# Performance work log

Hardware: AMD Instinct MI355X
Metric: run time of the kernel (lower is better)

Reference implementation:

```python
import jax, jax.numpy as jnp
import numpy as np

HIDDEN = 2048
NUM_HEADS = 16
NUM_KV_HEADS = 8
HEAD_DIM = 128
EPS = 1e-6
ROPE_THETA = 10000.0
SEQ = 2048
Q_SIZE = NUM_HEADS * HEAD_DIM
KV_SIZE = NUM_KV_HEADS * HEAD_DIM


def rmsnorm_f32(x, w, eps=EPS):
    # RMSNormF32: normalize in float32, scale by weight
    xf = x.astype(jnp.float32)
    var = jnp.mean(xf * xf, axis=-1, keepdims=True)
    return xf * jax.lax.rsqrt(var + eps) * w.astype(jnp.float32)


def apply_rope(x, cos, sin):
    # x: [S, H, D]; cos/sin: [S, D//2] (neox-style half split)
    half = x.shape[-1] // 2
    x1, x2 = x[..., :half], x[..., half:]
    c = cos[:, None, :]
    s = sin[:, None, :]
    return jnp.concatenate([x1 * c - x2 * s, x2 * c + x1 * s], axis=-1)


def setup_inputs() -> dict:
    key = jax.random.key(0)
    ks = jax.random.split(key, 6)
    return {
        "positions": jnp.arange(SEQ, dtype=jnp.int32),
        "hidden_states": jax.random.normal(ks[0], (SEQ, HIDDEN), jnp.float32),
        "ln_weight": 1.0 + 0.1 * jax.random.normal(ks[1], (HIDDEN,), jnp.float32),
        "qkv_weight": 0.02 * jax.random.normal(ks[2], (Q_SIZE + 2 * KV_SIZE, HIDDEN), jnp.float32),
        "q_norm_weight": 1.0 + 0.1 * jax.random.normal(ks[3], (HEAD_DIM,), jnp.float32),
        "k_norm_weight": 1.0 + 0.1 * jax.random.normal(ks[4], (HEAD_DIM,), jnp.float32),
        "o_weight": 0.02 * jax.random.normal(ks[5], (HIDDEN, Q_SIZE), jnp.float32),
    }


def reference(positions, hidden_states, ln_weight, qkv_weight, q_norm_weight, k_norm_weight, o_weight):
    S = hidden_states.shape[0]
    # 1. input RMSNorm (f32)
    normalized = rmsnorm_f32(hidden_states, ln_weight)
    # 2. fused QKV projection (no bias)
    qkv = normalized @ qkv_weight.T  # [S, q_size + 2*kv_size]
    q = qkv[:, :Q_SIZE].reshape(S, NUM_HEADS, HEAD_DIM)
    k = qkv[:, Q_SIZE:Q_SIZE + KV_SIZE].reshape(S, NUM_KV_HEADS, HEAD_DIM)
    v = qkv[:, Q_SIZE + KV_SIZE:].reshape(S, NUM_KV_HEADS, HEAD_DIM)
    # 3. RoPE (neox half-split, cache built from theta)
    inv_freq = ROPE_THETA ** (-jnp.arange(0, HEAD_DIM, 2, dtype=jnp.float32) / HEAD_DIM)
    freqs = positions.astype(jnp.float32)[:, None] * inv_freq[None, :]  # [S, D/2]
    cos, sin = jnp.cos(freqs), jnp.sin(freqs)
    q = apply_rope(q, cos, sin)
    k = apply_rope(k, cos, sin)
    # 4. per-head q/k RMSNorm (applied after RoPE, as in source)
    q = rmsnorm_f32(q, q_norm_weight)
    k = rmsnorm_f32(k, k_norm_weight)
    # 5. GQA expand kv heads
    rep = NUM_HEADS // NUM_KV_HEADS
    k = jnp.repeat(k, rep, axis=1)  # [S, NH, D]
    v = jnp.repeat(v, rep, axis=1)
    # 6. naive causal attention
    scores = jnp.einsum('shd,thd->hst', q, k) / (HEAD_DIM ** 0.5)  # [NH, S, S]
    causal = jnp.triu(jnp.ones((S, S), dtype=bool), k=1)
    scores = jnp.where(causal[None, :, :], -jnp.inf, scores)
    attn = jax.nn.softmax(scores, axis=-1)
    attn = jnp.nan_to_num(attn, nan=0.0)
    out = jnp.einsum('hst,thd->shd', attn, v).reshape(S, Q_SIZE)
    # 7. output projection
    return out @ o_weight.T
```

## Files before the change

kernel.cpp:

```cpp
#include <hip/hip_runtime.h>
#include <hip/hip_bf16.h>
#include <stdint.h>

typedef unsigned short u16;
typedef __attribute__((ext_vector_type(4))) float f32x4;
typedef __attribute__((ext_vector_type(8))) __bf16 bf16x8;
typedef __attribute__((ext_vector_type(8))) unsigned short u16x8;

#define SEQ 2048
#define HID 2048
#define HD  128

__device__ __forceinline__ float b2f(u16 v) {
    union { float f; unsigned u; } c; c.u = ((unsigned)v) << 16; return c.f;
}
__device__ __forceinline__ u16 f2b(float f) {
    union { float f; unsigned u; } c; c.f = f;
    unsigned r = c.u + 0x7fffu + ((c.u >> 16) & 1u);
    return (u16)(r >> 16);
}
__device__ __forceinline__ bf16x8 tob(u16x8 v) {
    union { u16x8 u; bf16x8 b; } c; c.u = v; return c.b;
}
__device__ __forceinline__ u16x8 ld8(const u16* p) { return *(const u16x8*)p; }

typedef const __attribute__((address_space(1))) unsigned int* gas_ptr;
typedef __attribute__((address_space(3))) unsigned int* las_ptr;
__device__ __forceinline__ void gld16(const void* g, void* l) {
    __builtin_amdgcn_global_load_lds((gas_ptr)g, (las_ptr)l, 16, 0, 0);
}

__global__ __launch_bounds__(256) void k_conv(const float* __restrict__ src,
                                              u16* __restrict__ dst) {
    const size_t i = ((size_t)blockIdx.x * 256 + threadIdx.x) * 8;
    f32x4 a = *(const f32x4*)(src + i);
    f32x4 b = *(const f32x4*)(src + i + 4);
    u16x8 o;
#pragma unroll
    for (int e = 0; e < 4; ++e) { o[e] = f2b(a[e]); o[e + 4] = f2b(b[e]); }
    *(u16x8*)(dst + i) = o;
}

__global__ __launch_bounds__(256) void k_rmsnorm(const float* __restrict__ x,
                                                 const float* __restrict__ w,
                                                 u16* __restrict__ o) {
    const int row = blockIdx.x, t = threadIdx.x;
    const float* xr = x + (size_t)row * HID + t * 8;
    f32x4 xa = *(const f32x4*)xr;
    f32x4 xb = *(const f32x4*)(xr + 4);
    float xf[8]; float ss = 0.f;
#pragma unroll
    for (int e = 0; e < 4; ++e) { xf[e] = xa[e]; xf[e + 4] = xb[e]; }
#pragma unroll
    for (int e = 0; e < 8; ++e) ss += xf[e] * xf[e];
#pragma unroll
    for (int m = 32; m; m >>= 1) ss += __shfl_xor(ss, m);
    __shared__ float red[4];
    if ((t & 63) == 0) red[t >> 6] = ss;
    __syncthreads();
    ss = red[0] + red[1] + red[2] + red[3];
    const float sc = rsqrtf(ss * (1.0f / HID) + 1e-6f);
    f32x4 wa = *(const f32x4*)(w + t * 8);
    f32x4 wb = *(const f32x4*)(w + t * 8 + 4);
    u16x8 ov;
#pragma unroll
    for (int e = 0; e < 4; ++e) {
        ov[e] = f2b(xf[e] * sc * wa[e]);
        ov[e + 4] = f2b(xf[e + 4] * sc * wb[e]);
    }
    *(u16x8*)(o + (size_t)row * HID + t * 8) = ov;
}

__global__ __launch_bounds__(256) void k_gemm_qkv(const u16* __restrict__ A,
                                                  const u16* __restrict__ B,
                                                  u16* __restrict__ qraw,
                                                  u16* __restrict__ kraw,
                                                  u16* __restrict__ vtr,
                                                  int K) {
    __shared__ u16 As[128 * 32];
    __shared__ u16 Bs[128 * 32];
    const int tid = threadIdx.x;
    const int wave = tid >> 6, lane = tid & 63, quad = lane >> 4, l16 = lane & 15;
    const int wm = wave >> 1, wn = wave & 1;
    const int m0 = blockIdx.x * 128, n0 = blockIdx.y * 128;
    f32x4 acc[4][4];
#pragma unroll
    for (int i = 0; i < 4; ++i)
#pragma unroll
        for (int j = 0; j < 4; ++j) acc[i][j] = (f32x4){0.f, 0.f, 0.f, 0.f};

    const u16* ga = A + (size_t)(m0 + (tid >> 2)) * K + (tid & 3) * 8;
    const u16* gb = B + (size_t)(n0 + (tid >> 2)) * K + (tid & 3) * 8;
    const size_t rowskip = (size_t)64 * K;
    char* lA = (char*)As + wave * 1024;
    char* lB = (char*)Bs + wave * 1024;

    for (int k0 = 0; k0 < K; k0 += 32) {
        gld16(ga + k0, lA);
        gld16(ga + k0 + rowskip, lA + 4096);
        gld16(gb + k0, lB);
        gld16(gb + k0 + rowskip, lB + 4096);
        __syncthreads();
        bf16x8 af[4], bfr[4];
#pragma unroll
        for (int i = 0; i < 4; ++i)
            af[i] = tob(ld8(As + (wm * 64 + i * 16 + l16) * 32 + quad * 8));
#pragma unroll
        for (int j = 0; j < 4; ++j)
            bfr[j] = tob(ld8(Bs + (wn * 64 + j * 16 + l16) * 32 + quad * 8));
#pragma unroll
        for (int i = 0; i < 4; ++i)
#pragma unroll
            for (int j = 0; j < 4; ++j)
                acc[i][j] = __builtin_amdgcn_mfma_f32_16x16x32_bf16(af[i], bfr[j], acc[i][j], 0, 0, 0);
        __syncthreads();
    }
#pragma unroll
    for (int i = 0; i < 4; ++i) {
        const int row = m0 + wm * 64 + i * 16 + quad * 4;
#pragma unroll
        for (int j = 0; j < 4; ++j) {
            const int col = n0 + wn * 64 + j * 16 + l16;
#pragma unroll
            for (int r = 0; r < 4; ++r) {
                const u16 val = f2b(acc[i][j][r]);
                const int s = row + r;
                if (col < 2048) {
                    const int head = col >> 7, d = col & 127;
                    qraw[((size_t)head * SEQ + s) * HD + d] = val;
                } else if (col < 3072) {
                    const int c = col - 2048, kv = c >> 7, d = c & 127;
                    kraw[((size_t)kv * SEQ + s) * HD + d] = val;
                } else {
                    const int c = col - 3072, kv = c >> 7, d = c & 127;
                    vtr[(size_t)kv * HD * SEQ + (size_t)d * SEQ + s] = val;
                }
            }
        }
    }
}

__global__ __launch_bounds__(256) void k_gemm_of(const u16* __restrict__ A,
                                                 const u16* __restrict__ B,
                                                 float* __restrict__ C,
                                                 int N, int K) {
    __shared__ u16 As[128 * 32];
    __shared__ u16 Bs[128 * 32];
    const int tid = threadIdx.x;
    const int wave = tid >> 6, lane = tid & 63, quad = lane >> 4, l16 = lane & 15;
    const int wm = wave >> 1, wn = wave & 1;
    const int m0 = blockIdx.x * 128, n0 = blockIdx.y * 128;
    f32x4 acc[4][4];
#pragma unroll
    for (int i = 0; i < 4; ++i)
#pragma unroll
        for (int j = 0; j < 4; ++j) acc[i][j] = (f32x4){0.f, 0.f, 0.f, 0.f};

    const u16* ga = A + (size_t)(m0 + (tid >> 2)) * K + (tid & 3) * 8;
    const u16* gb = B + (size_t)(n0 + (tid >> 2)) * K + (tid & 3) * 8;
    const size_t rowskip = (size_t)64 * K;
    char* lA = (char*)As + wave * 1024;
    char* lB = (char*)Bs + wave * 1024;

    for (int k0 = 0; k0 < K; k0 += 32) {
        gld16(ga + k0, lA);
        gld16(ga + k0 + rowskip, lA + 4096);
        gld16(gb + k0, lB);
        gld16(gb + k0 + rowskip, lB + 4096);
        __syncthreads();
        bf16x8 af[4], bfr[4];
#pragma unroll
        for (int i = 0; i < 4; ++i)
            af[i] = tob(ld8(As + (wm * 64 + i * 16 + l16) * 32 + quad * 8));
#pragma unroll
        for (int j = 0; j < 4; ++j)
            bfr[j] = tob(ld8(Bs + (wn * 64 + j * 16 + l16) * 32 + quad * 8));
#pragma unroll
        for (int i = 0; i < 4; ++i)
#pragma unroll
            for (int j = 0; j < 4; ++j)
                acc[i][j] = __builtin_amdgcn_mfma_f32_16x16x32_bf16(af[i], bfr[j], acc[i][j], 0, 0, 0);
        __syncthreads();
    }
#pragma unroll
    for (int i = 0; i < 4; ++i) {
        const int row = m0 + wm * 64 + i * 16 + quad * 4;
#pragma unroll
        for (int j = 0; j < 4; ++j) {
            const int col = n0 + wn * 64 + j * 16 + l16;
#pragma unroll
            for (int r = 0; r < 4; ++r)
                C[(size_t)(row + r) * N + col] = acc[i][j][r];
        }
    }
}

__global__ __launch_bounds__(256) void k_ropenorm(const int* __restrict__ pos,
                                                  const float* __restrict__ qw,
                                                  const float* __restrict__ kw,
                                                  u16* __restrict__ qraw,
                                                  u16* __restrict__ kraw) {
    const int s = blockIdx.x;
    const int h = blockIdx.y * 4 + (threadIdx.x >> 6);
    const int d = threadIdx.x & 63;
    const bool isq = h < 16;
    u16* row = isq ? (qraw + ((size_t)h * SEQ + s) * HD)
                   : (kraw + ((size_t)(h - 16) * SEQ + s) * HD);
    const float x1 = b2f(row[d]), x2 = b2f(row[d + 64]);
    const float p = (float)pos[s];
    const float inv = exp2f(-(float)d * (2.0f / 128.0f) * 13.287712379549449f);
    const float fr = p * inv;
    const float c = cosf(fr), sn = sinf(fr);
    const float o1 = x1 * c - x2 * sn;
    const float o2 = x2 * c + x1 * sn;
    float ss = o1 * o1 + o2 * o2;
#pragma unroll
    for (int m = 32; m; m >>= 1) ss += __shfl_xor(ss, m);
    const float sc = rsqrtf(ss * (1.0f / HD) + 1e-6f);
    const float* w = isq ? qw : kw;
    row[d] = f2b(o1 * sc * w[d]);
    row[d + 64] = f2b(o2 * sc * w[d + 64]);
}

__global__ __launch_bounds__(256) void k_attn(const u16* __restrict__ qh,
                                              const u16* __restrict__ kh,
                                              const u16* __restrict__ vt,
                                              u16* __restrict__ out) {
    const int tid = threadIdx.x;
    const int wave = tid >> 6, lane = tid & 63, quad = lane >> 4, l16 = lane & 15;
    const int head = blockIdx.y;
    const int bx = blockIdx.x;
    const int f = (bx & 1) ? 31 - (bx >> 1) : (bx >> 1);
    const int qt = (head < 8) ? f : 31 - f;
    const int kvh = head >> 1;
    const int q0 = qt * 64;

    __shared__ u16 Ks[64 * 128];
    __shared__ u16 Vts[128 * 64];
    __shared__ u16 Ps[4][16 * 64];

    const u16* qbase = qh + ((size_t)head * SEQ + q0 + wave * 16) * HD;
    bf16x8 aq[4];
#pragma unroll
    for (int kk = 0; kk < 4; ++kk)
        aq[kk] = tob(ld8(qbase + l16 * HD + kk * 32 + quad * 8));

    f32x4 acco[8];
#pragma unroll
    for (int j = 0; j < 8; ++j) acco[j] = (f32x4){0.f, 0.f, 0.f, 0.f};
    f32x4 lrow = (f32x4){0.f, 0.f, 0.f, 0.f};

    const float sc = 0.08838834764831845f;
    const u16* kbase = kh + (size_t)kvh * SEQ * HD;
    const u16* vbase = vt + (size_t)kvh * HD * SEQ;
    const int ntiles = qt + 1;
    u16* pw = &Ps[wave][0];

    const u16* kg0 = kbase + (size_t)tid * 8;
    const u16* vg0 = vbase + (size_t)(tid >> 3) * SEQ + (size_t)(tid & 7) * 8;
    int kst[4], vst[4];
#pragma unroll
    for (int r = 0; r < 4; ++r) {
        const int krow = r * 16 + (tid >> 4);
        kst[r] = krow * 128 + (((tid & 15) ^ (krow & 7)) << 3);
        const int vrow = r * 32 + (tid >> 3);
        vst[r] = vrow * 64 + (((tid & 7) ^ (vrow & 7)) << 3);
    }

    u16x8 kreg[4], vreg[4];
#pragma unroll
    for (int r = 0; r < 4; ++r) {
        kreg[r] = ld8(kg0 + (size_t)r * 2048);
        vreg[r] = ld8(vg0 + (size_t)r * 32 * SEQ);
    }
#pragma unroll
    for (int r = 0; r < 4; ++r) {
        *(u16x8*)(Ks + kst[r]) = kreg[r];
        *(u16x8*)(Vts + vst[r]) = vreg[r];
    }
    __syncthreads();

    for (int kt = 0; kt < ntiles; ++kt) {
        if (kt + 1 < ntiles) {
            const size_t koff = (size_t)(kt + 1) * 64;
#pragma unroll
            for (int r = 0; r < 4; ++r) {
                kreg[r] = ld8(kg0 + koff * HD + (size_t)r * 2048);
                vreg[r] = ld8(vg0 + koff + (size_t)r * 32 * SEQ);
            }
        }

        f32x4 accs[4];
#pragma unroll
        for (int j = 0; j < 4; ++j) accs[j] = (f32x4){0.f, 0.f, 0.f, 0.f};
#pragma unroll
        for (int kk = 0; kk < 4; ++kk) {
#pragma unroll
            for (int j = 0; j < 4; ++j) {
                const int krow = j * 16 + l16;
                const bf16x8 bk = tob(ld8(Ks + krow * 128 + (((kk * 4 + quad) ^ (krow & 7)) << 3)));
                accs[j] = __builtin_amdgcn_mfma_f32_16x16x32_bf16(aq[kk], bk, accs[j], 0, 0, 0);
            }
        }

        const int k0 = kt * 64;
        const int rowb = q0 + wave * 16 + quad * 4;
#pragma unroll
        for (int j = 0; j < 4; ++j) {
            const int col = k0 + j * 16 + l16;
#pragma unroll
            for (int r = 0; r < 4; ++r) {
                const float p = (col > rowb + r) ? 0.f : __expf(accs[j][r] * sc);
                lrow[r] += p;
                const int prow = quad * 4 + r;
                const int pcol = j * 16 + l16;
                pw[prow * 64 + ((((pcol >> 3) ^ (prow & 7)) << 3) | (pcol & 7))] = f2b(p);
            }
        }

        __syncthreads();

#pragma unroll
        for (int kk = 0; kk < 2; ++kk) {
            const bf16x8 ap = tob(ld8(pw + l16 * 64 + (((kk * 4 + quad) ^ (l16 & 7)) << 3)));
#pragma unroll
            for (int j = 0; j < 8; ++j) {
                const int vrow = j * 16 + l16;
                const bf16x8 bv = tob(ld8(Vts + vrow * 64 + (((kk * 4 + quad) ^ (vrow & 7)) << 3)));
                acco[j] = __builtin_amdgcn_mfma_f32_16x16x32_bf16(ap, bv, acco[j], 0, 0, 0);
            }
        }
        __syncthreads();

        if (kt + 1 < ntiles) {
#pragma unroll
            for (int r = 0; r < 4; ++r) {
                *(u16x8*)(Ks + kst[r]) = kreg[r];
                *(u16x8*)(Vts + vst[r]) = vreg[r];
            }
        }
        __syncthreads();
    }

    f32x4 il;
#pragma unroll
    for (int r = 0; r < 4; ++r) {
        float v = lrow[r];
        v += __shfl_xor(v, 1);
        v += __shfl_xor(v, 2);
        v += __shfl_xor(v, 4);
        v += __shfl_xor(v, 8);
        il[r] = 1.0f / v;
    }
    const int rowb = q0 + wave * 16 + quad * 4;
#pragma unroll
    for (int j = 0; j < 8; ++j) {
        const int col = head * HD + j * 16 + l16;
#pragma unroll
        for (int r = 0; r < 4; ++r)
            out[(size_t)(rowb + r) * 2048 + col] = f2b(acco[j][r] * il[r]);
    }
}

extern "C" void kernel_launch(void* const* d_in, const int* in_sizes, int n_in,
                              void* d_out, int out_size, void* d_ws, size_t ws_size,
                              hipStream_t stream) {
    const int*   positions = (const int*)d_in[0];
    const float* hidden   = (const float*)d_in[1];
    const float* lnw      = (const float*)d_in[2];
    const float* qkvw     = (const float*)d_in[3];
    const float* qnw      = (const float*)d_in[4];
    const float* knw      = (const float*)d_in[5];
    const float* ow       = (const float*)d_in[6];
    float* outp = (float*)d_out;

    char* ws = (char*)d_ws;
    const size_t MB = 1024ull * 1024ull;
    u16* normed = (u16*)(ws + 0 * MB);
    u16* qraw   = (u16*)(ws + 8 * MB);
    u16* kraw   = (u16*)(ws + 16 * MB);
    u16* vtr    = (u16*)(ws + 20 * MB);
    u16* qkvwb  = (u16*)(ws + 24 * MB);
    u16* owb    = (u16*)(ws + 0 * MB);
    u16* attno  = (u16*)(ws + 24 * MB);

    k_rmsnorm <<<SEQ, 256, 0, stream>>>(hidden, lnw, normed);
    k_conv    <<<4096, 256, 0, stream>>>(qkvw, qkvwb);
    k_gemm_qkv<<<dim3(16, 32), 256, 0, stream>>>(normed, qkvwb, qraw, kraw, vtr, HID);
    k_ropenorm<<<dim3(SEQ, 6), 256, 0, stream>>>(positions, qnw, knw, qraw, kraw);
    k_conv    <<<2048, 256, 0, stream>>>(ow, owb);
    k_attn    <<<dim3(32, 16), 256, 0, stream>>>(qraw, kraw, vtr, attno);
    k_gemm_of <<<dim3(16, 16), 256, 0, stream>>>(attno, owb, outp, HID, HID);
}
```

Before: 289.7 us.

## Double the GEMM K-step per barrier and double-buffer attention K/V tiles

In both GEMM kernels each iteration now loads two 32-wide K slices into separate LDS buffers and runs both MFMA batches under a single pair of barriers. This halves the barrier count per K. In attention, K and V tiles alternate between two LDS buffers, so the barrier before writing the next tile is removed. The cost is doubled LDS use per block, which can lower occupancy, and the GEMM still has no overlap between loads and compute inside an iteration.

```diff
diff --git a/kernel.cpp b/kernel.cpp
--- a/kernel.cpp
+++ b/kernel.cpp
@@ -77,8 +77,8 @@
                                                   u16* __restrict__ kraw,
                                                   u16* __restrict__ vtr,
                                                   int K) {
-    __shared__ u16 As[128 * 32];
-    __shared__ u16 Bs[128 * 32];
+    __shared__ u16 As[2][128 * 32];
+    __shared__ u16 Bs[2][128 * 32];
     const int tid = threadIdx.x;
     const int wave = tid >> 6, lane = tid & 63, quad = lane >> 4, l16 = lane & 15;
     const int wm = wave >> 1, wn = wave & 1;
@@ -92,27 +92,36 @@
     const u16* ga = A + (size_t)(m0 + (tid >> 2)) * K + (tid & 3) * 8;
     const u16* gb = B + (size_t)(n0 + (tid >> 2)) * K + (tid & 3) * 8;
     const size_t rowskip = (size_t)64 * K;
-    char* lA = (char*)As + wave * 1024;
-    char* lB = (char*)Bs + wave * 1024;
-
-    for (int k0 = 0; k0 < K; k0 += 32) {
-        gld16(ga + k0, lA);
-        gld16(ga + k0 + rowskip, lA + 4096);
-        gld16(gb + k0, lB);
-        gld16(gb + k0 + rowskip, lB + 4096);
-        __syncthreads();
-        bf16x8 af[4], bfr[4];
-#pragma unroll
-        for (int i = 0; i < 4; ++i)
-            af[i] = tob(ld8(As + (wm * 64 + i * 16 + l16) * 32 + quad * 8));
-#pragma unroll
-        for (int j = 0; j < 4; ++j)
-            bfr[j] = tob(ld8(Bs + (wn * 64 + j * 16 + l16) * 32 + quad * 8));
-#pragma unroll
-        for (int i = 0; i < 4; ++i)
+    char* lA0 = (char*)&As[0][0] + wave * 1024;
+    char* lA1 = (char*)&As[1][0] + wave * 1024;
+    char* lB0 = (char*)&Bs[0][0] + wave * 1024;
+    char* lB1 = (char*)&Bs[1][0] + wave * 1024;
+
+    for (int k0 = 0; k0 < K; k0 += 64) {
+        gld16(ga + k0, lA0);
+        gld16(ga + k0 + rowskip, lA0 + 4096);
+        gld16(ga + k0 + 32, lA1);
+        gld16(ga + k0 + 32 + rowskip, lA1 + 4096);
+        gld16(gb + k0, lB0);
+        gld16(gb + k0 + rowskip, lB0 + 4096);
+        gld16(gb + k0 + 32, lB1);
+        gld16(gb + k0 + 32 + rowskip, lB1 + 4096);
+        __syncthreads();
+#pragma unroll
+        for (int h = 0; h < 2; ++h) {
+            bf16x8 af[4], bfr[4];
+#pragma unroll
+            for (int i = 0; i < 4; ++i)
+                af[i] = tob(ld8(&As[h][0] + (wm * 64 + i * 16 + l16) * 32 + quad * 8));
 #pragma unroll
             for (int j = 0; j < 4; ++j)
-                acc[i][j] = __builtin_amdgcn_mfma_f32_16x16x32_bf16(af[i], bfr[j], acc[i][j], 0, 0, 0);
+                bfr[j] = tob(ld8(&Bs[h][0] + (wn * 64 + j * 16 + l16) * 32 + quad * 8));
+#pragma unroll
+            for (int i = 0; i < 4; ++i)
+#pragma unroll
+                for (int j = 0; j < 4; ++j)
+                    acc[i][j] = __builtin_amdgcn_mfma_f32_16x16x32_bf16(af[i], bfr[j], acc[i][j], 0, 0, 0);
+        }
         __syncthreads();
     }
 #pragma unroll
@@ -144,8 +153,8 @@
                                                  const u16* __restrict__ B,
                                                  float* __restrict__ C,
                                                  int N, int K) {
-    __shared__ u16 As[128 * 32];
-    __shared__ u16 Bs[128 * 32];
+    __shared__ u16 As[2][128 * 32];
+    __shared__ u16 Bs[2][128 * 32];
     const int tid = threadIdx.x;
     const int wave = tid >> 6, lane = tid & 63, quad = lane >> 4, l16 = lane & 15;
     const int wm = wave >> 1, wn = wave & 1;
@@ -159,27 +168,36 @@
     const u16* ga = A + (size_t)(m0 + (tid >> 2)) * K + (tid & 3) * 8;
     const u16* gb = B + (size_t)(n0 + (tid >> 2)) * K + (tid & 3) * 8;
     const size_t rowskip = (size_t)64 * K;
-    char* lA = (char*)As + wave * 1024;
-    char* lB = (char*)Bs + wave * 1024;
-
-    for (int k0 = 0; k0 < K; k0 += 32) {
-        gld16(ga + k0, lA);
-        gld16(ga + k0 + rowskip, lA + 4096);
-        gld16(gb + k0, lB);
-        gld16(gb + k0 + rowskip, lB + 4096);
-        __syncthreads();
-        bf16x8 af[4], bfr[4];
-#pragma unroll
-        for (int i = 0; i < 4; ++i)
-            af[i] = tob(ld8(As + (wm * 64 + i * 16 + l16) * 32 + quad * 8));
-#pragma unroll
-        for (int j = 0; j < 4; ++j)
-            bfr[j] = tob(ld8(Bs + (wn * 64 + j * 16 + l16) * 32 + quad * 8));
-#pragma unroll
-        for (int i = 0; i < 4; ++i)
+    char* lA0 = (char*)&As[0][0] + wave * 1024;
+    char* lA1 = (char*)&As[1][0] + wave * 1024;
+    char* lB0 = (char*)&Bs[0][0] + wave * 1024;
+    char* lB1 = (char*)&Bs[1][0] + wave * 1024;
+
+    for (int k0 = 0; k0 < K; k0 += 64) {
+        gld16(ga + k0, lA0);
+        gld16(ga + k0 + rowskip, lA0 + 4096);
+        gld16(ga + k0 + 32, lA1);
+        gld16(ga + k0 + 32 + rowskip, lA1 + 4096);
+        gld16(gb + k0, lB0);
+        gld16(gb + k0 + rowskip, lB0 + 4096);
+        gld16(gb + k0 + 32, lB1);
+        gld16(gb + k0 + 32 + rowskip, lB1 + 4096);
+        __syncthreads();
+#pragma unroll
+        for (int h = 0; h < 2; ++h) {
+            bf16x8 af[4], bfr[4];
+#pragma unroll
+            for (int i = 0; i < 4; ++i)
+                af[i] = tob(ld8(&As[h][0] + (wm * 64 + i * 16 + l16) * 32 + quad * 8));
 #pragma unroll
             for (int j = 0; j < 4; ++j)
-                acc[i][j] = __builtin_amdgcn_mfma_f32_16x16x32_bf16(af[i], bfr[j], acc[i][j], 0, 0, 0);
+                bfr[j] = tob(ld8(&Bs[h][0] + (wn * 64 + j * 16 + l16) * 32 + quad * 8));
+#pragma unroll
+            for (int i = 0; i < 4; ++i)
+#pragma unroll
+                for (int j = 0; j < 4; ++j)
+                    acc[i][j] = __builtin_amdgcn_mfma_f32_16x16x32_bf16(af[i], bfr[j], acc[i][j], 0, 0, 0);
+        }
         __syncthreads();
     }
 #pragma unroll
@@ -235,8 +253,8 @@
     const int kvh = head >> 1;
     const int q0 = qt * 64;
 
-    __shared__ u16 Ks[64 * 128];
-    __shared__ u16 Vts[128 * 64];
+    __shared__ u16 Ks[2][64 * 128];
+    __shared__ u16 Vts[2][128 * 64];
     __shared__ u16 Ps[4][16 * 64];
 
     const u16* qbase = qh + ((size_t)head * SEQ + q0 + wave * 16) * HD;
@@ -275,12 +293,16 @@
     }
 #pragma unroll
     for (int r = 0; r < 4; ++r) {
-        *(u16x8*)(Ks + kst[r]) = kreg[r];
-        *(u16x8*)(Vts + vst[r]) = vreg[r];
+        *(u16x8*)(&Ks[0][0] + kst[r]) = kreg[r];
+        *(u16x8*)(&Vts[0][0] + vst[r]) = vreg[r];
     }
     __syncthreads();
 
     for (int kt = 0; kt < ntiles; ++kt) {
+        const int cur = kt & 1;
+        const u16* ksc = &Ks[cur][0];
+        const u16* vsc = &Vts[cur][0];
+
         if (kt + 1 < ntiles) {
             const size_t koff = (size_t)(kt + 1) * 64;
 #pragma unroll
@@ -298,7 +320,7 @@
 #pragma unroll
             for (int j = 0; j < 4; ++j) {
                 const int krow = j * 16 + l16;
-                const bf16x8 bk = tob(ld8(Ks + krow * 128 + (((kk * 4 + quad) ^ (krow & 7)) << 3)));
+                const bf16x8 bk = tob(ld8(ksc + krow * 128 + (((kk * 4 + quad) ^ (krow & 7)) << 3)));
                 accs[j] = __builtin_amdgcn_mfma_f32_16x16x32_bf16(aq[kk], bk, accs[j], 0, 0, 0);
             }
         }
@@ -326,17 +348,18 @@
 #pragma unroll
             for (int j = 0; j < 8; ++j) {
                 const int vrow = j * 16 + l16;
-                const bf16x8 bv = tob(ld8(Vts + vrow * 64 + (((kk * 4 + quad) ^ (vrow & 7)) << 3)));
+                const bf16x8 bv = tob(ld8(vsc + vrow * 64 + (((kk * 4 + quad) ^ (vrow & 7)) << 3)));
                 acco[j] = __builtin_amdgcn_mfma_f32_16x16x32_bf16(ap, bv, acco[j], 0, 0, 0);
             }
         }
-        __syncthreads();
 
         if (kt + 1 < ntiles) {
+            u16* ksn = &Ks[1 - cur][0];
+            u16* vsn = &Vts[1 - cur][0];
 #pragma unroll
             for (int r = 0; r < 4; ++r) {
-                *(u16x8*)(Ks + kst[r]) = kreg[r];
-                *(u16x8*)(Vts + vst[r]) = vreg[r];
+                *(u16x8*)(ksn + kst[r]) = kreg[r];
+                *(u16x8*)(vsn + vst[r]) = vreg[r];
             }
         }
         __syncthreads();
```

After: 274.1 us. 1.06x faster.
